# Kernel optimization log

Hardware: AMD Instinct MI355X
Metric: run time of the kernel (lower is better)

The kernel has to match this reference:

```python
import jax, jax.numpy as jnp
import numpy as np

B, S, MEM, D, H = 4, 1024, 1024, 1024, 16
T = S + MEM          # total_len (memory + current segment)
DK = D // H          # 64


def setup_inputs() -> dict:
    key = jax.random.key(0)
    ks = jax.random.split(key, 12)
    wscale = 1.0 / np.sqrt(D).astype(np.float32)
    q = jax.random.normal(ks[0], (B, S, D), jnp.float32)
    k = jax.random.normal(ks[1], (B, T, D), jnp.float32)
    v = jax.random.normal(ks[2], (B, T, D), jnp.float32)
    u = jax.random.normal(ks[3], (1, H, 1, DK), jnp.float32)
    v_bias = jax.random.normal(ks[4], (1, H, 1, DK), jnp.float32)
    Wq = jax.random.normal(ks[5], (D, D), jnp.float32) * wscale
    Wk = jax.random.normal(ks[6], (D, D), jnp.float32) * wscale
    Wv = jax.random.normal(ks[7], (D, D), jnp.float32) * wscale
    Wr = jax.random.normal(ks[8], (D, D), jnp.float32) * wscale
    Wo = jax.random.normal(ks[9], (D, D), jnp.float32) * wscale
    R = jax.random.normal(ks[10], (T, D), jnp.float32)  # positional encodings
    # TXL causal mask: query i may attend to keys j <= i + MEM
    causal = jnp.tril(jnp.ones((S, T), jnp.bool_), k=MEM)
    mask = jnp.broadcast_to(causal[None], (B, S, T))
    return {"q": q, "k": k, "v": v, "mask": mask, "u": u, "v_bias": v_bias,
            "Wq": Wq, "Wk": Wk, "Wv": Wv, "Wr": Wr, "Wo": Wo, "R": R}


def circulant_shift(x, shift):
    # Matches torch: gather cols with idx[i, j] = (roll(arange(W), shift)[j] + i) % W
    h, w = x.shape[-2], x.shape[-1]
    idx = (jnp.roll(jnp.arange(w), shift)[None, :] + jnp.arange(h)[:, None]) % w
    return jnp.take_along_axis(x, idx[None, None], axis=-1)


def reference(q, k, v, mask, u, v_bias, Wq, Wk, Wv, Wr, Wo, R):
    # projections (nn.Linear: y = x @ W.T), split heads -> [B, H, L, DK]
    qh = (q @ Wq.T).reshape(B, S, H, DK).transpose(0, 2, 1, 3)
    kh = (k @ Wk.T).reshape(B, T, H, DK).transpose(0, 2, 1, 3)
    vh = (v @ Wv.T).reshape(B, T, H, DK).transpose(0, 2, 1, 3)
    rh = (R[-T:] @ Wr.T).reshape(1, T, H, DK).transpose(0, 2, 1, 3)
    ac = jnp.einsum('bhid,bhjd->bhij', qh + u, kh)         # content term
    bd = jnp.einsum('bhid,bhjd->bhij', qh + v_bias, rh)    # position term
    bd = circulant_shift(bd, -S + 1)
    score = (ac + bd) / np.sqrt(DK).astype(np.float32)
    score = jnp.where(mask[:, None], score, -jnp.inf)      # mask==0 -> -inf
    att = jax.nn.softmax(score, axis=-1)                   # dropout p=0
    o = jnp.einsum('bhij,bhjd->bhid', att, vh)             # [B, H, S, DK]
    concat = o.transpose(0, 2, 1, 3).reshape(B, S, D)
    return concat @ Wo.T
```

## Files before the change

kernel.cpp:

```cpp
#include <hip/hip_runtime.h>
#include <hip/hip_bf16.h>
#include <stdint.h>

#define Ss   1024
#define MEMm 1024
#define Tt   2048
#define Dd   1024
#define Hh   16
#define DKk  64

typedef unsigned short u16;
using f32x4 = __attribute__((ext_vector_type(4))) float;
using s16x8 = __attribute__((ext_vector_type(8))) short;

__device__ __forceinline__ u16 f2bf(float x) {
  __hip_bfloat16 h = __float2bfloat16(x);
  return *(reinterpret_cast<u16*>(&h));
}
__device__ __forceinline__ float b2f(short s) {
  union { uint32_t u; float f; } c; c.u = ((uint32_t)(u16)s) << 16; return c.f;
}
__device__ __forceinline__ uint32_t pk2(float lo, float hi) {
  return (uint32_t)f2bf(lo) | ((uint32_t)f2bf(hi) << 16);
}
__device__ __forceinline__ f32x4 mfma16(s16x8 a, s16x8 b, f32x4 c) {
  return __builtin_amdgcn_mfma_f32_16x16x32_bf16(a, b, c, 0, 0, 0);
}
__device__ __forceinline__ void gl_lds16(const u16* g, u16* l) {
  __builtin_amdgcn_global_load_lds(
      (const __attribute__((address_space(1))) uint32_t*)g,
      (__attribute__((address_space(3))) uint32_t*)l, 16, 0, 0);
}

__global__ __launch_bounds__(256)
void cvt7(const float* __restrict__ w0, const float* __restrict__ w1,
          const float* __restrict__ w2, const float* __restrict__ w3,
          const float* __restrict__ w4, const float* __restrict__ kk,
          const float* __restrict__ vv, u16* __restrict__ Wb,
          u16* __restrict__ kd, u16* __restrict__ vd) {
  const float* s;
  u16* d;
  int n8;
  switch (blockIdx.y) {
    case 0: s = w0; d = Wb;                     n8 = 131072;  break;
    case 1: s = w1; d = Wb + ((size_t)1 << 20); n8 = 131072;  break;
    case 2: s = w2; d = Wb + ((size_t)2 << 20); n8 = 131072;  break;
    case 3: s = w3; d = Wb + ((size_t)3 << 20); n8 = 131072;  break;
    case 4: s = w4; d = Wb + ((size_t)4 << 20); n8 = 131072;  break;
    case 5: s = kk; d = kd;                     n8 = 1048576; break;
    default: s = vv; d = vd;                    n8 = 1048576; break;
  }
  int i = blockIdx.x * 256 + threadIdx.x;
  const int stride = gridDim.x * 256;
  for (; i < n8; i += stride) {
    const float4* p = (const float4*)(s + (size_t)i * 8);
    const float4 a = p[0], bq = p[1];
    uint4 o;
    o.x = pk2(a.x, a.y);   o.y = pk2(a.z, a.w);
    o.z = pk2(bq.x, bq.y); o.w = pk2(bq.z, bq.w);
    *(uint4*)(d + (size_t)i * 8) = o;
  }
}

template <int EPI>
__device__ __forceinline__
void gemm_epi(f32x4 (&acc)[4][4], void* __restrict__ O, int n0, int m0) {
  const int lane = threadIdx.x & 63, wave = threadIdx.x >> 6;
  const int fr = lane & 15, fq = lane >> 4;
  const int wr = (wave >> 1) * 64, wc = (wave & 1) * 64;
#pragma unroll
  for (int i = 0; i < 4; ++i)
#pragma unroll
    for (int j = 0; j < 4; ++j) {
      if constexpr (EPI == 2) {
        const int grow = n0 + wr + i * 16 + fq * 4;
        const int m = m0 + wc + j * 16 + fr;
        const int bb = grow >> 11, t = grow & 2047;
        const int hh = m >> 6, dk = m & 63;
        ushort4 pk4;
        pk4.x = f2bf(acc[i][j][0]); pk4.y = f2bf(acc[i][j][1]);
        pk4.z = f2bf(acc[i][j][2]); pk4.w = f2bf(acc[i][j][3]);
        *(ushort4*)&((u16*)O)[(((size_t)(bb * Hh + hh) * DKk + dk) << 11) + t] = pk4;
      } else {
#pragma unroll
        for (int r = 0; r < 4; ++r) {
          const int n = n0 + wr + i * 16 + fq * 4 + r;
          const int m = m0 + wc + j * 16 + fr;
          const float y = acc[i][j][r];
          if constexpr (EPI == 0) {
            const int bb = n >> 10, s = n & 1023, hh = m >> 6, dk = m & 63;
            ((u16*)O)[((size_t)(bb * Hh + hh) * Ss + s) * DKk + dk] = f2bf(y);
          } else if constexpr (EPI == 1) {
            const int bb = n >> 11, t = n & 2047, hh = m >> 6, dk = m & 63;
            ((u16*)O)[((size_t)(bb * Hh + hh) * Tt + t) * DKk + dk] = f2bf(y);
          } else if constexpr (EPI == 3) {
            const int hh = m >> 6, dk = m & 63;
            ((u16*)O)[((size_t)hh * Tt + n) * DKk + dk] = f2bf(y);
          } else {
            ((float*)O)[(size_t)n * Dd + m] = y;
          }
        }
      }
    }
}

template <int EPI>
__device__ __forceinline__
void gemm_body(const u16* __restrict__ X, const u16* __restrict__ W,
               void* __restrict__ O, int n0, int m0, u16* As, u16* Bs) {
  const int tid = threadIdx.x;
  const int lane = tid & 63, wave = tid >> 6;
  const int fr = lane & 15, fq = lane >> 4;
  const int wr = (wave >> 1) * 64, wc = (wave & 1) * 64;
  f32x4 acc[4][4] = {};

  const int lrow = lane >> 2, lcol = (lane & 3) * 8;
  const u16* xg0 = X + (size_t)(n0 + wave * 16 + lrow) * Dd + lcol;
  const u16* xg1 = X + (size_t)(n0 + 64 + wave * 16 + lrow) * Dd + lcol;
  const u16* wg0 = W + (size_t)(m0 + wave * 16 + lrow) * Dd + lcol;
  const u16* wg1 = W + (size_t)(m0 + 64 + wave * 16 + lrow) * Dd + lcol;
  u16* la0 = &As[(wave * 16) * 32];
  u16* la1 = &As[(64 + wave * 16) * 32];
  u16* lb0 = &Bs[(wave * 16) * 32];
  u16* lb1 = &Bs[(64 + wave * 16) * 32];

  for (int k0 = 0; k0 < Dd; k0 += 32) {
    gl_lds16(xg0 + k0, la0);
    gl_lds16(xg1 + k0, la1);
    gl_lds16(wg0 + k0, lb0);
    gl_lds16(wg1 + k0, lb1);
    __syncthreads();
    s16x8 af[4], bfv[4];
#pragma unroll
    for (int i = 0; i < 4; ++i)
      af[i] = *(const s16x8*)&As[(wr + i * 16 + fr) * 32 + fq * 8];
#pragma unroll
    for (int j = 0; j < 4; ++j)
      bfv[j] = *(const s16x8*)&Bs[(wc + j * 16 + fr) * 32 + fq * 8];
#pragma unroll
    for (int i = 0; i < 4; ++i)
#pragma unroll
      for (int j = 0; j < 4; ++j)
        acc[i][j] = mfma16(af[i], bfv[j], acc[i][j]);
    __syncthreads();
  }
  gemm_epi<EPI>(acc, O, n0, m0);
}

template <int EPI>
__device__ __forceinline__
void gemm_body_f32(const float* __restrict__ X, const u16* __restrict__ W,
                   void* __restrict__ O, int n0, int m0, u16* As, u16* Bs) {
  const int tid = threadIdx.x;
  const int lane = tid & 63, wave = tid >> 6;
  const int fr = lane & 15, fq = lane >> 4;
  const int wr = (wave >> 1) * 64, wc = (wave & 1) * 64;
  f32x4 acc[4][4] = {};

  const int arow = tid >> 1, acol = (tid & 1) * 16;
  const float* xg = X + (size_t)(n0 + arow) * Dd + acol;
  u16* aw = &As[arow * 32 + acol];

  const int lrow = lane >> 2, lcol = (lane & 3) * 8;
  const u16* wg0 = W + (size_t)(m0 + wave * 16 + lrow) * Dd + lcol;
  const u16* wg1 = W + (size_t)(m0 + 64 + wave * 16 + lrow) * Dd + lcol;
  u16* lb0 = &Bs[(wave * 16) * 32];
  u16* lb1 = &Bs[(64 + wave * 16) * 32];

  for (int k0 = 0; k0 < Dd; k0 += 32) {
    const float4 f0 = *(const float4*)(xg + k0);
    const float4 f1 = *(const float4*)(xg + k0 + 4);
    const float4 f2 = *(const float4*)(xg + k0 + 8);
    const float4 f3 = *(const float4*)(xg + k0 + 12);
    __syncthreads();
    gl_lds16(wg0 + k0, lb0);
    gl_lds16(wg1 + k0, lb1);
    uint4 p0, p1;
    p0.x = pk2(f0.x, f0.y); p0.y = pk2(f0.z, f0.w);
    p0.z = pk2(f1.x, f1.y); p0.w = pk2(f1.z, f1.w);
    p1.x = pk2(f2.x, f2.y); p1.y = pk2(f2.z, f2.w);
    p1.z = pk2(f3.x, f3.y); p1.w = pk2(f3.z, f3.w);
    *(uint4*)aw = p0;
    *(uint4*)(aw + 8) = p1;
    __syncthreads();
    s16x8 af[4], bfv[4];
#pragma unroll
    for (int i = 0; i < 4; ++i)
      af[i] = *(const s16x8*)&As[(wr + i * 16 + fr) * 32 + fq * 8];
#pragma unroll
    for (int j = 0; j < 4; ++j)
      bfv[j] = *(const s16x8*)&Bs[(wc + j * 16 + fr) * 32 + fq * 8];
#pragma unroll
    for (int i = 0; i < 4; ++i)
#pragma unroll
      for (int j = 0; j < 4; ++j)
        acc[i][j] = mfma16(af[i], bfv[j], acc[i][j]);
  }
  gemm_epi<EPI>(acc, O, n0, m0);
}

__global__ __launch_bounds__(256)
void gemm_all(const u16* __restrict__ kstg, const u16* __restrict__ vstg,
              const float* __restrict__ qf, const float* __restrict__ Rf,
              const u16* __restrict__ Wb,
              u16* __restrict__ QH, u16* __restrict__ KH,
              u16* __restrict__ VT, u16* __restrict__ RH) {
  __shared__ u16 As[128 * 32];
  __shared__ u16 Bs[128 * 32];
  const int bid = blockIdx.x;
  if (bid < 512) {
    const int t = bid;
    gemm_body<1>(kstg, Wb + ((size_t)1 << 20), KH,
                 (t >> 3) * 128, (t & 7) * 128, As, Bs);
  } else if (bid < 1024) {
    const int t = bid - 512;
    gemm_body<2>(vstg, Wb + ((size_t)2 << 20), VT,
                 (t >> 3) * 128, (t & 7) * 128, As, Bs);
  } else if (bid < 1280) {
    const int t = bid - 1024;
    gemm_body_f32<0>(qf, Wb, QH, (t >> 3) * 128, (t & 7) * 128, As, Bs);
  } else {
    const int t = bid - 1280;
    gemm_body_f32<3>(Rf, Wb + ((size_t)3 << 20), RH,
                     (t >> 3) * 128, (t & 7) * 128, As, Bs);
  }
}

__global__ __launch_bounds__(256)
void gemm_o(const u16* __restrict__ X, const u16* __restrict__ W,
            float* __restrict__ O) {
  __shared__ u16 As[128 * 32];
  __shared__ u16 Bs[128 * 32];
  const int tid = threadIdx.x;
  const int lane = tid & 63, wave = tid >> 6;
  (void)lane; (void)wave;
  gemm_body<4>(X, W, O, blockIdx.x * 128, blockIdx.y * 128, As, Bs);
}

__global__ __launch_bounds__(256, 2)
void attn7(const u16* __restrict__ QH, const u16* __restrict__ KH,
           const u16* __restrict__ VT, const u16* __restrict__ RH,
           const float* __restrict__ ub, const float* __restrict__ vbb,
           u16* __restrict__ CONCAT) {
  __shared__ u16 Ks[64 * 64];
  __shared__ u16 Vt[64 * 64];
  __shared__ u16 RB[256 * 64];
  __shared__ u16 Pl[4][2][16 * 72];

  const int tid = threadIdx.x;
  const int wave = tid >> 6, lane = tid & 63;
  const int fr = lane & 15, fq = lane >> 4;

  const int wid = blockIdx.x;
  const int bx = (wid < 256) ? (wid >> 6) : (11 - (wid >> 6));
  const int bh = wid & 63;
  const int h = bh & 15, b = bh >> 4;
  const int i0 = bx * 128;
  const int r0 = i0 + wave * 32;
  const int nch = 2 * bx + 18;
  const int base = (i0 + 1023) & 2047;

  const u16* qB  = QH + (size_t)bh * (Ss * DKk);
  const u16* khB = KH + (size_t)bh * (Tt * DKk);
  const u16* vtB = VT + (size_t)bh * (DKk * Tt);
  const u16* rhB = RH + (size_t)h * (Tt * DKk);

  float ulo[8], uhi[8], vlo[8], vhi[8];
  {
    const float* up = ub + h * 64 + fq * 8;
    const float* vp = vbb + h * 64 + fq * 8;
    *(float4*)&ulo[0] = *(const float4*)up;
    *(float4*)&ulo[4] = *(const float4*)(up + 4);
    *(float4*)&uhi[0] = *(const float4*)(up + 32);
    *(float4*)&uhi[4] = *(const float4*)(up + 36);
    *(float4*)&vlo[0] = *(const float4*)vp;
    *(float4*)&vlo[4] = *(const float4*)(vp + 4);
    *(float4*)&vhi[0] = *(const float4*)(vp + 32);
    *(float4*)&vhi[4] = *(const float4*)(vp + 36);
  }

  s16x8 qu[2][2], qv[2][2];
#pragma unroll
  for (int s = 0; s < 2; ++s) {
    const u16* qp = qB + (size_t)(r0 + s * 16 + fr) * DKk + fq * 8;
    const s16x8 q0 = *(const s16x8*)qp;
    const s16x8 q1 = *(const s16x8*)(qp + 32);
    union U8 { s16x8 v; uint32_t w[4]; } a0, a1, c0, c1;
#pragma unroll
    for (int e = 0; e < 4; ++e) {
      a0.w[e] = pk2(b2f(q0[2*e]) + ulo[2*e], b2f(q0[2*e+1]) + ulo[2*e+1]);
      a1.w[e] = pk2(b2f(q1[2*e]) + uhi[2*e], b2f(q1[2*e+1]) + uhi[2*e+1]);
      c0.w[e] = pk2(b2f(q0[2*e]) + vlo[2*e], b2f(q0[2*e+1]) + vlo[2*e+1]);
      c1.w[e] = pk2(b2f(q1[2*e]) + vhi[2*e], b2f(q1[2*e+1]) + vhi[2*e+1]);
    }
    qu[s][0] = a0.v; qu[s][1] = a1.v; qv[s][0] = c0.v; qv[s][1] = c1.v;
  }

  s16x8 vone;
  {
    union U8 { s16x8 v; uint32_t w[4]; } o;
    const uint32_t f = (fr == 0) ? 0x3F803F80u : 0u;
#pragma unroll
    for (int e = 0; e < 4; ++e) o.w[e] = f;
    vone = o.v;
  }

  const int srow = lane >> 3, sch = lane & 7;
  const int row0 = wave * 8 + srow;
  const int row1 = wave * 8 + 32 + srow;
  const int swc = (sch ^ srow) * 8;

#pragma unroll
  for (int p = 0; p < 6; ++p) {
    const int off = p * 32 + wave * 8 + srow;
    const uint4 rr =
        *(const uint4*)(rhB + (size_t)((base + off) & 2047) * 64 + swc);
    *(uint4*)&RB[off * 64 + sch * 8] = rr;
  }
  {
    const uint4 k0 = *(const uint4*)(khB + (size_t)row0 * 64 + swc);
    const uint4 k1 = *(const uint4*)(khB + (size_t)row1 * 64 + swc);
    const uint4 v0 = *(const uint4*)(vtB + (size_t)row0 * Tt + swc);
    const uint4 v1 = *(const uint4*)(vtB + (size_t)row1 * Tt + swc);
    *(uint4*)&Ks[row0 * 64 + sch * 8] = k0;
    *(uint4*)&Ks[row1 * 64 + sch * 8] = k1;
    *(uint4*)&Vt[row0 * 64 + sch * 8] = v0;
    *(uint4*)&Vt[row1 * 64 + sch * 8] = v1;
  }

  f32x4 oacc[2][4] = {};
  f32x4 oacc2[2] = {};
  float mrun[2][4];
#pragma unroll
  for (int s = 0; s < 2; ++s)
#pragma unroll
    for (int r = 0; r < 4; ++r) mrun[s][r] = -1e30f;

  const float SC = 0.18033688011f;
  const float THR = 11.0f;

  for (int c = 0; c < nch; ++c) {
    const int j0 = c * 64;
    const bool more = (c + 1 < nch);
    __syncthreads();

    uint4 kr0, kr1, vr0, vr1;
    if (more) {
      kr0 = *(const uint4*)(khB + (size_t)(j0 + 64 + row0) * 64 + swc);
      kr1 = *(const uint4*)(khB + (size_t)(j0 + 64 + row1) * 64 + swc);
      vr0 = *(const uint4*)(vtB + (size_t)row0 * Tt + (j0 + 64) + swc);
      vr1 = *(const uint4*)(vtB + (size_t)row1 * Tt + (j0 + 64) + swc);
    }
    const int offA0 = j0 + 192 + wave * 8 + srow;
    const int offA1 = offA0 + 32;
    const uint4 rr0 =
        *(const uint4*)(rhB + (size_t)((base + offA0) & 2047) * 64 + swc);
    const uint4 rr1 =
        *(const uint4*)(rhB + (size_t)((base + offA1) & 2047) * 64 + swc);

    s16x8 rf[6][2];
#pragma unroll
    for (int mt = 0; mt < 6; ++mt) {
      const int rho = (j0 + wave * 32 + mt * 16 + fr) & 255;
#pragma unroll
      for (int hh = 0; hh < 2; ++hh)
        rf[mt][hh] = *(const s16x8*)&RB[rho * 64 + (((hh * 4 + fq) ^ (rho & 7)) * 8)];
    }

    f32x4 g[2][5];
    __builtin_amdgcn_s_setprio(1);
#pragma unroll
    for (int s = 0; s < 2; ++s)
#pragma unroll
      for (int k = 0; k < 5; ++k) {
        f32x4 t = {};
        t = mfma16(qv[s][0], rf[s + k][0], t);
        t = mfma16(qv[s][1], rf[s + k][1], t);
        g[s][k] = t;
      }
    __builtin_amdgcn_s_setprio(0);

    s16x8 kf[4][2];
#pragma unroll
    for (int ct = 0; ct < 4; ++ct) {
      const int row = ct * 16 + fr;
#pragma unroll
      for (int hh = 0; hh < 2; ++hh)
        kf[ct][hh] = *(const s16x8*)&Ks[row * 64 + (((hh * 4 + fq) ^ (row & 7)) * 8)];
    }

    f32x4 pacc[2][4];
#pragma unroll
    for (int s = 0; s < 2; ++s) {
#pragma unroll
      for (int r = 0; r < 4; ++r) {
        const int sum = fq * 4 + r + fr;
        const int src = fq * 16 + (sum & 15);
        const bool cy = sum >= 16;
        const float s0 = __shfl(g[s][0][r], src);
        const float s1 = __shfl(g[s][1][r], src);
        const float s2 = __shfl(g[s][2][r], src);
        const float s3 = __shfl(g[s][3][r], src);
        const float s4 = __shfl(g[s][4][r], src);
        pacc[s][0][r] = cy ? s1 : s0;
        pacc[s][1][r] = cy ? s2 : s1;
        pacc[s][2][r] = cy ? s3 : s2;
        pacc[s][3][r] = cy ? s4 : s3;
      }
    }
    __builtin_amdgcn_s_setprio(1);
#pragma unroll
    for (int s = 0; s < 2; ++s)
#pragma unroll
      for (int ct = 0; ct < 4; ++ct) {
        pacc[s][ct] = mfma16(qu[s][0], kf[ct][0], pacc[s][ct]);
        pacc[s][ct] = mfma16(qu[s][1], kf[ct][1], pacc[s][ct]);
      }
    __builtin_amdgcn_s_setprio(0);

#pragma unroll
    for (int s = 0; s < 2; ++s) {
      const int rbase = r0 + s * 16;
      if (j0 + 63 > rbase + MEMm) {
#pragma unroll
        for (int ct = 0; ct < 4; ++ct)
#pragma unroll
          for (int r = 0; r < 4; ++r) {
            const int gi = rbase + fq * 4 + r, gj = j0 + ct * 16 + fr;
            const float vv = pacc[s][ct][r] * SC;
            pacc[s][ct][r] = (gj > gi + MEMm) ? -1e30f : vv;
          }
      } else {
#pragma unroll
        for (int ct = 0; ct < 4; ++ct)
#pragma unroll
          for (int r = 0; r < 4; ++r) pacc[s][ct][r] *= SC;
      }
      float cm[4];
#pragma unroll
      for (int r = 0; r < 4; ++r) {
        float t = fmaxf(fmaxf(pacc[s][0][r], pacc[s][1][r]),
                        fmaxf(pacc[s][2][r], pacc[s][3][r]));
        int v = __builtin_bit_cast(int, t);
        int t2 = __builtin_amdgcn_update_dpp(v, v, 0xB1, 0xF, 0xF, true);
        t = fmaxf(t, __builtin_bit_cast(float, t2)); v = __builtin_bit_cast(int, t);
        t2 = __builtin_amdgcn_update_dpp(v, v, 0x4E, 0xF, 0xF, true);
        t = fmaxf(t, __builtin_bit_cast(float, t2)); v = __builtin_bit_cast(int, t);
        t2 = __builtin_amdgcn_update_dpp(v, v, 0x141, 0xF, 0xF, true);
        t = fmaxf(t, __builtin_bit_cast(float, t2)); v = __builtin_bit_cast(int, t);
        t2 = __builtin_amdgcn_update_dpp(v, v, 0x140, 0xF, 0xF, true);
        t = fmaxf(t, __builtin_bit_cast(float, t2));
        cm[r] = t;
      }
      bool need = false;
#pragma unroll
      for (int r = 0; r < 4; ++r) need = need || (cm[r] > mrun[s][r] + THR);
      if (__any(need)) {
        float alpha[4];
#pragma unroll
        for (int r = 0; r < 4; ++r) {
          const float mn = fmaxf(mrun[s][r], cm[r]);
          alpha[r] = exp2f(mrun[s][r] - mn);
          mrun[s][r] = mn;
        }
#pragma unroll
        for (int t = 0; t < 4; ++t)
#pragma unroll
          for (int r = 0; r < 4; ++r) oacc[s][t][r] *= alpha[r];
#pragma unroll
        for (int r = 0; r < 4; ++r) oacc2[s][r] *= alpha[r];
      }
#pragma unroll
      for (int ct = 0; ct < 4; ++ct)
#pragma unroll
        for (int r = 0; r < 4; ++r)
          pacc[s][ct][r] = exp2f(pacc[s][ct][r] - mrun[s][r]);
    }

#pragma unroll
    for (int s = 0; s < 2; ++s)
#pragma unroll
      for (int ct = 0; ct < 4; ++ct)
#pragma unroll
        for (int r = 0; r < 4; ++r)
          Pl[wave][s][(fq * 4 + r) * 72 + ct * 16 + fr] = f2bf(pacc[s][ct][r]);
    asm volatile("s_waitcnt lgkmcnt(0)" ::: "memory");
    __builtin_amdgcn_sched_barrier(0);
    s16x8 ap[2][2];
#pragma unroll
    for (int s = 0; s < 2; ++s)
#pragma unroll
      for (int hh = 0; hh < 2; ++hh)
        ap[s][hh] = *(const s16x8*)&Pl[wave][s][fr * 72 + hh * 32 + fq * 8];

    s16x8 vf[4][2];
#pragma unroll
    for (int nt = 0; nt < 4; ++nt) {
      const int row = nt * 16 + fr;
#pragma unroll
      for (int hh = 0; hh < 2; ++hh)
        vf[nt][hh] = *(const s16x8*)&Vt[row * 64 + (((hh * 4 + fq) ^ (row & 7)) * 8)];
    }
    __builtin_amdgcn_s_setprio(1);
#pragma unroll
    for (int s = 0; s < 2; ++s) {
#pragma unroll
      for (int nt = 0; nt < 4; ++nt) {
        oacc[s][nt] = mfma16(ap[s][0], vf[nt][0], oacc[s][nt]);
        oacc[s][nt] = mfma16(ap[s][1], vf[nt][1], oacc[s][nt]);
      }
      oacc2[s] = mfma16(ap[s][0], vone, oacc2[s]);
      oacc2[s] = mfma16(ap[s][1], vone, oacc2[s]);
    }
    __builtin_amdgcn_s_setprio(0);

    __syncthreads();
    if (more) {
      *(uint4*)&Ks[row0 * 64 + sch * 8] = kr0;
      *(uint4*)&Ks[row1 * 64 + sch * 8] = kr1;
      *(uint4*)&Vt[row0 * 64 + sch * 8] = vr0;
      *(uint4*)&Vt[row1 * 64 + sch * 8] = vr1;
    }
    *(uint4*)&RB[(offA0 & 255) * 64 + sch * 8] = rr0;
    *(uint4*)&RB[(offA1 & 255) * 64 + sch * 8] = rr1;
  }

#pragma unroll
  for (int s = 0; s < 2; ++s) {
    float linv[4];
#pragma unroll
    for (int r = 0; r < 4; ++r)
      linv[r] = 1.0f / __shfl(oacc2[s][r], lane & 48);
#pragma unroll
    for (int nt = 0; nt < 4; ++nt)
#pragma unroll
      for (int r = 0; r < 4; ++r) {
        const int gi = r0 + s * 16 + fq * 4 + r;
        CONCAT[((size_t)b * Ss + gi) * Dd + h * DKk + nt * 16 + fr] =
            f2bf(oacc[s][nt][r] * linv[r]);
      }
  }
}

extern "C" void kernel_launch(void* const* d_in, const int* in_sizes, int n_in,
                              void* d_out, int out_size, void* d_ws,
                              size_t ws_size, hipStream_t stream) {
  (void)in_sizes; (void)n_in; (void)out_size; (void)ws_size;
  const float* q  = (const float*)d_in[0];
  const float* k  = (const float*)d_in[1];
  const float* v  = (const float*)d_in[2];
  const float* u  = (const float*)d_in[4];
  const float* vb = (const float*)d_in[5];
  const float* Wq = (const float*)d_in[6];
  const float* Wk = (const float*)d_in[7];
  const float* Wv = (const float*)d_in[8];
  const float* Wr = (const float*)d_in[9];
  const float* Wo = (const float*)d_in[10];
  const float* R  = (const float*)d_in[11];

  char* ws = (char*)d_ws;
  u16* QH  = (u16*)ws; ws += 8388608;
  u16* KH  = (u16*)ws; ws += 16777216;
  u16* VT  = (u16*)ws; ws += 16777216;
  u16* RH  = (u16*)ws; ws += 4194304;
  u16* Wb  = (u16*)ws; ws += 10485760;
  u16* STG = (u16*)ws;

  const size_t M1 = (size_t)1 << 20;
  u16* kstg = STG;
  u16* vstg = STG + ((size_t)8 << 20);

  cvt7<<<dim3(512, 7), 256, 0, stream>>>(Wq, Wk, Wv, Wr, Wo, k, v,
                                         Wb, kstg, vstg);
  gemm_all<<<1408, 256, 0, stream>>>(kstg, vstg, q, R, Wb, QH, KH, VT, RH);
  attn7<<<512, 256, 0, stream>>>(QH, KH, VT, RH, u, vb, STG);
  gemm_o<<<dim3(32, 8), 256, 0, stream>>>(STG, Wb + 4 * M1, (float*)d_out);
}
```

Before: 241.6 us.

## Pipeline positional-score MFMAs across iterations and widen GEMM K-tile with swizzle

In the attention kernel, the position-term (BD) MFMAs and their shuffle-based circulant shift for the next chunk now run at the end of the current iteration. The global loads of the next R rows are also issued later, so the score phase at the top of each iteration depends less on fresh loads. The projection GEMMs stage a 64-wide K tile instead of 32, using an XOR LDS swizzle, which halves the barriers per K step. Both GEMM kernels now request two blocks per CU through their launch bounds. The BD reads of RB now happen right after the RB writes with no barrier between them, which risks a race on shared memory.

Measured after the change: 228.8 us. 5.3% less time.

```diff
diff --git a/kernel.cpp b/kernel.cpp
--- a/kernel.cpp
+++ b/kernel.cpp
@@ -114,34 +114,37 @@
   const int wr = (wave >> 1) * 64, wc = (wave & 1) * 64;
   f32x4 acc[4][4] = {};
 
-  const int lrow = lane >> 2, lcol = (lane & 3) * 8;
-  const u16* xg0 = X + (size_t)(n0 + wave * 16 + lrow) * Dd + lcol;
-  const u16* xg1 = X + (size_t)(n0 + 64 + wave * 16 + lrow) * Dd + lcol;
-  const u16* wg0 = W + (size_t)(m0 + wave * 16 + lrow) * Dd + lcol;
-  const u16* wg1 = W + (size_t)(m0 + 64 + wave * 16 + lrow) * Dd + lcol;
-  u16* la0 = &As[(wave * 16) * 32];
-  u16* la1 = &As[(64 + wave * 16) * 32];
-  u16* lb0 = &Bs[(wave * 16) * 32];
-  u16* lb1 = &Bs[(64 + wave * 16) * 32];
-
-  for (int k0 = 0; k0 < Dd; k0 += 32) {
-    gl_lds16(xg0 + k0, la0);
-    gl_lds16(xg1 + k0, la1);
-    gl_lds16(wg0 + k0, lb0);
-    gl_lds16(wg1 + k0, lb1);
+  const int lrow8 = lane >> 3;
+  const int lcol  = (lane & 7) * 8;
+
+  for (int k0 = 0; k0 < Dd; k0 += 64) {
+#pragma unroll
+    for (int p = 0; p < 4; ++p) {
+      const int row = p * 32 + wave * 8 + lrow8;
+      const int scol = lcol ^ ((row & 1) * 32);
+      gl_lds16(X + (size_t)(n0 + row) * Dd + k0 + scol, &As[(p * 32 + wave * 8) * 64]);
+      gl_lds16(W + (size_t)(m0 + row) * Dd + k0 + scol, &Bs[(p * 32 + wave * 8) * 64]);
+    }
     __syncthreads();
-    s16x8 af[4], bfv[4];
-#pragma unroll
-    for (int i = 0; i < 4; ++i)
-      af[i] = *(const s16x8*)&As[(wr + i * 16 + fr) * 32 + fq * 8];
-#pragma unroll
-    for (int j = 0; j < 4; ++j)
-      bfv[j] = *(const s16x8*)&Bs[(wc + j * 16 + fr) * 32 + fq * 8];
-#pragma unroll
-    for (int i = 0; i < 4; ++i)
-#pragma unroll
-      for (int j = 0; j < 4; ++j)
-        acc[i][j] = mfma16(af[i], bfv[j], acc[i][j]);
+#pragma unroll
+    for (int kc = 0; kc < 2; ++kc) {
+      s16x8 af[4], bfv[4];
+#pragma unroll
+      for (int i = 0; i < 4; ++i) {
+        const int row = wr + i * 16 + fr;
+        af[i] = *(const s16x8*)&As[row * 64 + ((kc * 32 + fq * 8) ^ ((row & 1) * 32))];
+      }
+#pragma unroll
+      for (int j = 0; j < 4; ++j) {
+        const int row = wc + j * 16 + fr;
+        bfv[j] = *(const s16x8*)&Bs[row * 64 + ((kc * 32 + fq * 8) ^ ((row & 1) * 32))];
+      }
+#pragma unroll
+      for (int i = 0; i < 4; ++i)
+#pragma unroll
+        for (int j = 0; j < 4; ++j)
+          acc[i][j] = mfma16(af[i], bfv[j], acc[i][j]);
+    }
     __syncthreads();
   }
   gemm_epi<EPI>(acc, O, n0, m0);
@@ -199,14 +202,14 @@
   gemm_epi<EPI>(acc, O, n0, m0);
 }
 
-__global__ __launch_bounds__(256)
+__global__ __launch_bounds__(256, 2)
 void gemm_all(const u16* __restrict__ kstg, const u16* __restrict__ vstg,
               const float* __restrict__ qf, const float* __restrict__ Rf,
               const u16* __restrict__ Wb,
               u16* __restrict__ QH, u16* __restrict__ KH,
               u16* __restrict__ VT, u16* __restrict__ RH) {
-  __shared__ u16 As[128 * 32];
-  __shared__ u16 Bs[128 * 32];
+  __shared__ u16 As[128 * 64];
+  __shared__ u16 Bs[128 * 64];
   const int bid = blockIdx.x;
   if (bid < 512) {
     const int t = bid;
@@ -226,22 +229,19 @@
   }
 }
 
-__global__ __launch_bounds__(256)
+__global__ __launch_bounds__(256, 2)
 void gemm_o(const u16* __restrict__ X, const u16* __restrict__ W,
             float* __restrict__ O) {
-  __shared__ u16 As[128 * 32];
-  __shared__ u16 Bs[128 * 32];
-  const int tid = threadIdx.x;
-  const int lane = tid & 63, wave = tid >> 6;
-  (void)lane; (void)wave;
+  __shared__ u16 As[128 * 64];
+  __shared__ u16 Bs[128 * 64];
   gemm_body<4>(X, W, O, blockIdx.x * 128, blockIdx.y * 128, As, Bs);
 }
 
 __global__ __launch_bounds__(256, 2)
-void attn7(const u16* __restrict__ QH, const u16* __restrict__ KH,
-           const u16* __restrict__ VT, const u16* __restrict__ RH,
-           const float* __restrict__ ub, const float* __restrict__ vbb,
-           u16* __restrict__ CONCAT) {
+void attn12(const u16* __restrict__ QH, const u16* __restrict__ KH,
+            const u16* __restrict__ VT, const u16* __restrict__ RH,
+            const float* __restrict__ ub, const float* __restrict__ vbb,
+            u16* __restrict__ CONCAT) {
   __shared__ u16 Ks[64 * 64];
   __shared__ u16 Vt[64 * 64];
   __shared__ u16 RB[256 * 64];
@@ -310,6 +310,47 @@
   const int row1 = wave * 8 + 32 + srow;
   const int swc = (sch ^ srow) * 8;
 
+  f32x4 pacc[2][4];
+
+  auto computeBD = [&](int jw) {
+    s16x8 rf[6][2];
+#pragma unroll
+    for (int mt = 0; mt < 6; ++mt) {
+      const int rho = (jw + wave * 32 + mt * 16 + fr) & 255;
+#pragma unroll
+      for (int hh = 0; hh < 2; ++hh)
+        rf[mt][hh] = *(const s16x8*)&RB[rho * 64 + (((hh * 4 + fq) ^ (rho & 7)) * 8)];
+    }
+#pragma unroll
+    for (int s = 0; s < 2; ++s) {
+      f32x4 g[5];
+      __builtin_amdgcn_s_setprio(1);
+#pragma unroll
+      for (int k2 = 0; k2 < 5; ++k2) {
+        f32x4 t = {};
+        t = mfma16(qv[s][0], rf[s + k2][0], t);
+        t = mfma16(qv[s][1], rf[s + k2][1], t);
+        g[k2] = t;
+      }
+      __builtin_amdgcn_s_setprio(0);
+#pragma unroll
+      for (int r = 0; r < 4; ++r) {
+        const int sum = fq * 4 + r + fr;
+        const int src = fq * 16 + (sum & 15);
+        const bool cy = sum >= 16;
+        const float s0 = __shfl(g[0][r], src);
+        const float s1 = __shfl(g[1][r], src);
+        const float s2 = __shfl(g[2][r], src);
+        const float s3 = __shfl(g[3][r], src);
+        const float s4 = __shfl(g[4][r], src);
+        pacc[s][0][r] = cy ? s1 : s0;
+        pacc[s][1][r] = cy ? s2 : s1;
+        pacc[s][2][r] = cy ? s3 : s2;
+        pacc[s][3][r] = cy ? s4 : s3;
+      }
+    }
+  };
+
 #pragma unroll
   for (int p = 0; p < 6; ++p) {
     const int off = p * 32 + wave * 8 + srow;
@@ -327,6 +368,8 @@
     *(uint4*)&Vt[row0 * 64 + sch * 8] = v0;
     *(uint4*)&Vt[row1 * 64 + sch * 8] = v1;
   }
+  __syncthreads();
+  computeBD(0);
 
   f32x4 oacc[2][4] = {};
   f32x4 oacc2[2] = {};
@@ -351,34 +394,6 @@
       vr0 = *(const uint4*)(vtB + (size_t)row0 * Tt + (j0 + 64) + swc);
       vr1 = *(const uint4*)(vtB + (size_t)row1 * Tt + (j0 + 64) + swc);
     }
-    const int offA0 = j0 + 192 + wave * 8 + srow;
-    const int offA1 = offA0 + 32;
-    const uint4 rr0 =
-        *(const uint4*)(rhB + (size_t)((base + offA0) & 2047) * 64 + swc);
-    const uint4 rr1 =
-        *(const uint4*)(rhB + (size_t)((base + offA1) & 2047) * 64 + swc);
-
-    s16x8 rf[6][2];
-#pragma unroll
-    for (int mt = 0; mt < 6; ++mt) {
-      const int rho = (j0 + wave * 32 + mt * 16 + fr) & 255;
-#pragma unroll
-      for (int hh = 0; hh < 2; ++hh)
-        rf[mt][hh] = *(const s16x8*)&RB[rho * 64 + (((hh * 4 + fq) ^ (rho & 7)) * 8)];
-    }
-
-    f32x4 g[2][5];
-    __builtin_amdgcn_s_setprio(1);
-#pragma unroll
-    for (int s = 0; s < 2; ++s)
-#pragma unroll
-      for (int k = 0; k < 5; ++k) {
-        f32x4 t = {};
-        t = mfma16(qv[s][0], rf[s + k][0], t);
-        t = mfma16(qv[s][1], rf[s + k][1], t);
-        g[s][k] = t;
-      }
-    __builtin_amdgcn_s_setprio(0);
 
     s16x8 kf[4][2];
 #pragma unroll
@@ -387,26 +402,6 @@
 #pragma unroll
       for (int hh = 0; hh < 2; ++hh)
         kf[ct][hh] = *(const s16x8*)&Ks[row * 64 + (((hh * 4 + fq) ^ (row & 7)) * 8)];
-    }
-
-    f32x4 pacc[2][4];
-#pragma unroll
-    for (int s = 0; s < 2; ++s) {
-#pragma unroll
-      for (int r = 0; r < 4; ++r) {
-        const int sum = fq * 4 + r + fr;
-        const int src = fq * 16 + (sum & 15);
-        const bool cy = sum >= 16;
-        const float s0 = __shfl(g[s][0][r], src);
-        const float s1 = __shfl(g[s][1][r], src);
-        const float s2 = __shfl(g[s][2][r], src);
-        const float s3 = __shfl(g[s][3][r], src);
-        const float s4 = __shfl(g[s][4][r], src);
-        pacc[s][0][r] = cy ? s1 : s0;
-        pacc[s][1][r] = cy ? s2 : s1;
-        pacc[s][2][r] = cy ? s3 : s2;
-        pacc[s][3][r] = cy ? s4 : s3;
-      }
     }
     __builtin_amdgcn_s_setprio(1);
 #pragma unroll
@@ -477,6 +472,13 @@
           pacc[s][ct][r] = exp2f(pacc[s][ct][r] - mrun[s][r]);
     }
 
+    const int offA0 = j0 + 192 + wave * 8 + srow;
+    const int offA1 = offA0 + 32;
+    const uint4 rr0 =
+        *(const uint4*)(rhB + (size_t)((base + offA0) & 2047) * 64 + swc);
+    const uint4 rr1 =
+        *(const uint4*)(rhB + (size_t)((base + offA1) & 2047) * 64 + swc);
+
 #pragma unroll
     for (int s = 0; s < 2; ++s)
 #pragma unroll
@@ -523,6 +525,8 @@
     }
     *(uint4*)&RB[(offA0 & 255) * 64 + sch * 8] = rr0;
     *(uint4*)&RB[(offA1 & 255) * 64 + sch * 8] = rr1;
+
+    if (more) computeBD(j0 + 64);
   }
 
 #pragma unroll
@@ -573,6 +577,6 @@
   cvt7<<<dim3(512, 7), 256, 0, stream>>>(Wq, Wk, Wv, Wr, Wo, k, v,
                                          Wb, kstg, vstg);
   gemm_all<<<1408, 256, 0, stream>>>(kstg, vstg, q, R, Wb, QH, KH, VT, RH);
-  attn7<<<512, 256, 0, stream>>>(QH, KH, VT, RH, u, vb, STG);
+  attn12<<<512, 256, 0, stream>>>(QH, KH, VT, RH, u, vb, STG);
   gemm_o<<<dim3(32, 8), 256, 0, stream>>>(STG, Wb + 4 * M1, (float*)d_out);
 }
```
